# Kernel tuning notes

Measured on AMD Instinct MI355X. Metric: run time of the kernel, lower is better.

## Reference

```python
import jax, jax.numpy as jnp
import numpy as np


def setup_inputs() -> dict:
    key = jax.random.key(0)
    k1, k2 = jax.random.split(key)
    B, S, D = 4, 2048, 1024
    x = jax.random.normal(k1, (B, S, D), dtype=jnp.float32)
    # uniform initializer in keras is small; scale to keep softmax well-behaved
    kernel = jax.random.normal(k2, (3, D, D), dtype=jnp.float32) * 0.02
    return {"x": x, "kernel": kernel}


def reference(x, kernel):
    # x: [B, S, D], kernel: [3, D, D]
    D = x.shape[-1]
    q = jnp.einsum('bsd,de->bse', x, kernel[0])
    k = jnp.einsum('bsd,de->bse', x, kernel[1])
    v = jnp.einsum('bsd,de->bse', x, kernel[2])
    scores = jnp.einsum('bqe,bke->bqk', q, k) / jnp.sqrt(jnp.float32(D))
    attn = jax.nn.softmax(scores, axis=-1)
    return jnp.einsum('bqk,bke->bqe', attn, v)
```

## Files before the change

### kernel.cpp

```cpp
#include <hip/hip_runtime.h>
#include <hip/hip_bf16.h>
#include <cstdint>

typedef __bf16 bf16x8 __attribute__((ext_vector_type(8)));
typedef float f32x4 __attribute__((ext_vector_type(4)));

__device__ __forceinline__ unsigned short f2bf(float f) {
  union { float f; uint32_t u; } a; a.f = f;
  uint32_t r = a.u + 0x7fffu + ((a.u >> 16) & 1u);
  return (unsigned short)(r >> 16);
}
__device__ __forceinline__ void gload_lds16(const unsigned short* g, unsigned short* l) {
  __builtin_amdgcn_global_load_lds(
      (const __attribute__((address_space(1))) void*)g,
      (__attribute__((address_space(3))) void*)l, 16, 0, 0);
}

__global__ void cast_all(const float* __restrict__ x, const float* __restrict__ W,
                         unsigned short* __restrict__ xb, unsigned short* __restrict__ Wt) {
  __shared__ float tile[32][33];
  const int bx = blockIdx.x;
  const int t = threadIdx.x;
  if (bx < 4096) {
    size_t i = ((size_t)bx * 256 + t) * 8;
    float4 a = *(const float4*)(x + i);
    float4 b = *(const float4*)(x + i + 4);
    uint4 o;
    o.x = (uint32_t)f2bf(a.x) | ((uint32_t)f2bf(a.y) << 16);
    o.y = (uint32_t)f2bf(a.z) | ((uint32_t)f2bf(a.w) << 16);
    o.z = (uint32_t)f2bf(b.x) | ((uint32_t)f2bf(b.y) << 16);
    o.w = (uint32_t)f2bf(b.z) | ((uint32_t)f2bf(b.w) << 16);
    *(uint4*)(xb + i) = o;
  } else {
    const int b = bx - 4096;
    const int z = b >> 10;
    const int rest = b & 1023;
    const int bxx = rest & 31, byy = rest >> 5;
    const float* Wz = W + (size_t)z * 1048576;
    unsigned short* Wtz = Wt + (size_t)z * 1048576;
    const int x0 = bxx * 32, y0 = byy * 32;
    const int tx = t & 31, ty = t >> 5;
#pragma unroll
    for (int i = 0; i < 32; i += 8)
      tile[ty + i][tx] = Wz[(size_t)(y0 + ty + i) * 1024 + x0 + tx];
    __syncthreads();
#pragma unroll
    for (int i = 0; i < 32; i += 8)
      Wtz[(size_t)(x0 + ty + i) * 1024 + y0 + tx] = f2bf(tile[tx][ty + i]);
  }
}

template <int MODE>
__global__ void __launch_bounds__(256)
gemm_bt(const unsigned short* __restrict__ Aall,
        const unsigned short* __restrict__ Btall,
        void* __restrict__ Call, unsigned short* __restrict__ VtPtr,
        float* __restrict__ aux,
        int K, int ldc, long sA, long sB, long sC, float scale) {
  __shared__ unsigned short As[2][4096];
  __shared__ unsigned short Bs[2][4096];
  const int t = threadIdx.x;
  const int lane = t & 63;
  const int quad = lane >> 4;
  const int l15 = lane & 15;
  const int wave = t >> 6;
  const int wm = (wave >> 1) * 64;
  const int wn = (wave & 1) * 64;
  const int z = blockIdx.z;

  const unsigned short* A = Aall + (size_t)z * sA + (size_t)blockIdx.x * 128 * K;
  const unsigned short* Bt = Btall + (size_t)z * sB + (size_t)blockIdx.y * 128 * K;

  const int srow = t >> 2;
  const int scol = (((t & 3) ^ ((srow >> 1) & 3)) * 8);
  const unsigned short* ga = A + (size_t)srow * K + scol;
  const unsigned short* gb = Bt + (size_t)srow * K + scol;
  const size_t rowskip = (size_t)64 * K;

  const int aOff = (wm + l15) * 32 + (quad ^ ((l15 >> 1) & 3)) * 8;
  const int bOff = (wn + l15) * 32 + (quad ^ ((l15 >> 1) & 3)) * 8;

  f32x4 acc[4][4];
#pragma unroll
  for (int i = 0; i < 4; i++)
#pragma unroll
    for (int j = 0; j < 4; j++) acc[i][j] = (f32x4){0.f, 0.f, 0.f, 0.f};

  gload_lds16(ga, &As[0][t * 8]);
  gload_lds16(ga + rowskip, &As[0][2048 + t * 8]);
  gload_lds16(gb, &Bs[0][t * 8]);
  gload_lds16(gb + rowskip, &Bs[0][2048 + t * 8]);

  int buf = 0;
  for (int k0 = 0; k0 < K; k0 += 32, buf ^= 1) {
    __syncthreads();
    if (k0 + 32 < K) {
      const int kn = k0 + 32;
      gload_lds16(ga + kn, &As[buf ^ 1][t * 8]);
      gload_lds16(ga + rowskip + kn, &As[buf ^ 1][2048 + t * 8]);
      gload_lds16(gb + kn, &Bs[buf ^ 1][t * 8]);
      gload_lds16(gb + rowskip + kn, &Bs[buf ^ 1][2048 + t * 8]);
    }
    const unsigned short* aB = &As[buf][aOff];
    const unsigned short* bB = &Bs[buf][bOff];
    bf16x8 a[4], b[4];
#pragma unroll
    for (int i = 0; i < 4; i++) a[i] = *(const bf16x8*)(aB + i * 512);
#pragma unroll
    for (int j = 0; j < 4; j++) b[j] = *(const bf16x8*)(bB + j * 512);
#pragma unroll
    for (int i = 0; i < 4; i++)
#pragma unroll
      for (int j = 0; j < 4; j++)
        acc[i][j] = __builtin_amdgcn_mfma_f32_16x16x32_bf16(a[i], b[j], acc[i][j], 0, 0, 0);
  }

  const int mbase = blockIdx.x * 128 + wm + quad * 4;
  const int nbase = blockIdx.y * 128 + wn + l15;

  if (MODE == 4) {
    if (z < 2) {
      unsigned short* C = (unsigned short*)Call + (size_t)z * sC;
#pragma unroll
      for (int mi = 0; mi < 4; mi++)
#pragma unroll
        for (int ni = 0; ni < 4; ni++) {
          const int m = mbase + mi * 16, n = nbase + ni * 16;
#pragma unroll
          for (int r = 0; r < 4; r++)
            C[(size_t)(m + r) * ldc + n] = f2bf(acc[mi][ni][r]);
        }
    } else {
      unsigned short* C = VtPtr;
#pragma unroll
      for (int mi = 0; mi < 4; mi++) {
        const int m = mbase + mi * 16;
        const int b = m >> 11, s = m & 2047;
#pragma unroll
        for (int ni = 0; ni < 4; ni++) {
          const int n = nbase + ni * 16;
          uint2 val;
          val.x = (uint32_t)f2bf(acc[mi][ni][0]) | ((uint32_t)f2bf(acc[mi][ni][1]) << 16);
          val.y = (uint32_t)f2bf(acc[mi][ni][2]) | ((uint32_t)f2bf(acc[mi][ni][3]) << 16);
          *(uint2*)(C + (size_t)b * 2097152 + (size_t)n * 2048 + s) = val;
        }
      }
    }
  } else if (MODE == 5) {
    unsigned short* C = (unsigned short*)Call + (size_t)z * sC;
    const int j = blockIdx.y * 2 + (wn >> 6);
#pragma unroll
    for (int mi = 0; mi < 4; mi++) {
#pragma unroll
      for (int r = 0; r < 4; r++) {
        const int m = mbase + mi * 16 + r;
        float s = 0.f;
#pragma unroll
        for (int ni = 0; ni < 4; ni++) {
          const float e = __expf(acc[mi][ni][r] * scale);
          C[(size_t)m * ldc + nbase + ni * 16] = f2bf(e);
          s += e;
        }
        s += __shfl_xor(s, 1);
        s += __shfl_xor(s, 2);
        s += __shfl_xor(s, 4);
        s += __shfl_xor(s, 8);
        if (l15 == 0) aux[(size_t)j * 8192 + (size_t)z * 2048 + m] = s;
      }
    }
  } else {
    float* C = (float*)Call + (size_t)z * sC;
#pragma unroll
    for (int mi = 0; mi < 4; mi++) {
#pragma unroll
      for (int r = 0; r < 4; r++) {
        const int m = mbase + mi * 16 + r;
        const size_t grow = (size_t)z * 2048 + m;
        float tot = 0.f;
#pragma unroll
        for (int j = 0; j < 32; j++) tot += aux[(size_t)j * 8192 + grow];
        const float inv = 1.f / tot;
#pragma unroll
        for (int ni = 0; ni < 4; ni++)
          C[(size_t)m * ldc + nbase + ni * 16] = acc[mi][ni][r] * inv;
      }
    }
  }
}

extern "C" void kernel_launch(void* const* d_in, const int* in_sizes, int n_in,
                              void* d_out, int out_size, void* d_ws, size_t ws_size,
                              hipStream_t stream) {
  const float* x = (const float*)d_in[0];
  const float* W = (const float*)d_in[1];
  float* out = (float*)d_out;
  char* ws = (char*)d_ws;
  unsigned short* xb = (unsigned short*)(ws);
  unsigned short* Wt = (unsigned short*)(ws + (16ll << 20));
  float* partial     = (float*)(ws + (16ll << 20));
  unsigned short* Q  = (unsigned short*)(ws + (22ll << 20));
  unsigned short* Kb = (unsigned short*)(ws + (38ll << 20));
  unsigned short* Vt = (unsigned short*)(ws + (54ll << 20));
  unsigned short* Sb = (unsigned short*)(ws + (70ll << 20));

  cast_all<<<7168, 256, 0, stream>>>(x, W, xb, Wt);

  gemm_bt<4><<<dim3(64, 8, 3), 256, 0, stream>>>(
      xb, Wt, Q, Vt, nullptr, 1024, 1024, 0L, 1048576L, 8388608L, 1.0f);
  gemm_bt<5><<<dim3(16, 16, 4), 256, 0, stream>>>(
      Q, Kb, Sb, nullptr, partial, 1024, 2048, 2097152L, 2097152L, 4194304L, 0.03125f);
  gemm_bt<6><<<dim3(16, 8, 4), 256, 0, stream>>>(
      Sb, Vt, out, nullptr, partial, 2048, 1024, 4194304L, 2097152L, 2097152L, 1.0f);
}
```

Baseline: 263.4 us.

## Fuse all attention stages into one cooperative persistent kernel with grid syncs

```diff
diff --git a/kernel.cpp b/kernel.cpp
--- a/kernel.cpp
+++ b/kernel.cpp
@@ -1,9 +1,17 @@
 #include <hip/hip_runtime.h>
+#include <hip/hip_cooperative_groups.h>
 #include <hip/hip_bf16.h>
 #include <cstdint>
 
+namespace cg = cooperative_groups;
+
 typedef __bf16 bf16x8 __attribute__((ext_vector_type(8)));
 typedef float f32x4 __attribute__((ext_vector_type(4)));
+
+struct SharedMem {
+  unsigned short As[2][4096];
+  unsigned short Bs[2][4096];
+};
 
 __device__ __forceinline__ unsigned short f2bf(float f) {
   union { float f; uint32_t u; } a; a.f = f;
@@ -16,60 +24,17 @@
       (__attribute__((address_space(3))) void*)l, 16, 0, 0);
 }
 
-__global__ void cast_all(const float* __restrict__ x, const float* __restrict__ W,
-                         unsigned short* __restrict__ xb, unsigned short* __restrict__ Wt) {
-  __shared__ float tile[32][33];
-  const int bx = blockIdx.x;
-  const int t = threadIdx.x;
-  if (bx < 4096) {
-    size_t i = ((size_t)bx * 256 + t) * 8;
-    float4 a = *(const float4*)(x + i);
-    float4 b = *(const float4*)(x + i + 4);
-    uint4 o;
-    o.x = (uint32_t)f2bf(a.x) | ((uint32_t)f2bf(a.y) << 16);
-    o.y = (uint32_t)f2bf(a.z) | ((uint32_t)f2bf(a.w) << 16);
-    o.z = (uint32_t)f2bf(b.x) | ((uint32_t)f2bf(b.y) << 16);
-    o.w = (uint32_t)f2bf(b.z) | ((uint32_t)f2bf(b.w) << 16);
-    *(uint4*)(xb + i) = o;
-  } else {
-    const int b = bx - 4096;
-    const int z = b >> 10;
-    const int rest = b & 1023;
-    const int bxx = rest & 31, byy = rest >> 5;
-    const float* Wz = W + (size_t)z * 1048576;
-    unsigned short* Wtz = Wt + (size_t)z * 1048576;
-    const int x0 = bxx * 32, y0 = byy * 32;
-    const int tx = t & 31, ty = t >> 5;
-#pragma unroll
-    for (int i = 0; i < 32; i += 8)
-      tile[ty + i][tx] = Wz[(size_t)(y0 + ty + i) * 1024 + x0 + tx];
-    __syncthreads();
-#pragma unroll
-    for (int i = 0; i < 32; i += 8)
-      Wtz[(size_t)(x0 + ty + i) * 1024 + y0 + tx] = f2bf(tile[tx][ty + i]);
-  }
-}
-
-template <int MODE>
-__global__ void __launch_bounds__(256)
-gemm_bt(const unsigned short* __restrict__ Aall,
-        const unsigned short* __restrict__ Btall,
-        void* __restrict__ Call, unsigned short* __restrict__ VtPtr,
-        float* __restrict__ aux,
-        int K, int ldc, long sA, long sB, long sC, float scale) {
-  __shared__ unsigned short As[2][4096];
-  __shared__ unsigned short Bs[2][4096];
+template <int NJ>
+__device__ __forceinline__ void gemm_tile_core(
+    const unsigned short* __restrict__ A, const unsigned short* __restrict__ Bt,
+    int K, SharedMem& sh, f32x4 (&acc)[4][NJ]) {
   const int t = threadIdx.x;
   const int lane = t & 63;
   const int quad = lane >> 4;
   const int l15 = lane & 15;
   const int wave = t >> 6;
   const int wm = (wave >> 1) * 64;
-  const int wn = (wave & 1) * 64;
-  const int z = blockIdx.z;
-
-  const unsigned short* A = Aall + (size_t)z * sA + (size_t)blockIdx.x * 128 * K;
-  const unsigned short* Bt = Btall + (size_t)z * sB + (size_t)blockIdx.y * 128 * K;
+  const int wn = (wave & 1) * (NJ * 16);
 
   const int srow = t >> 2;
   const int scol = (((t & 3) ^ ((srow >> 1) & 3)) * 8);
@@ -77,50 +42,104 @@
   const unsigned short* gb = Bt + (size_t)srow * K + scol;
   const size_t rowskip = (size_t)64 * K;
 
-  const int aOff = (wm + l15) * 32 + (quad ^ ((l15 >> 1) & 3)) * 8;
-  const int bOff = (wn + l15) * 32 + (quad ^ ((l15 >> 1) & 3)) * 8;
-
-  f32x4 acc[4][4];
+  const int swz = (quad ^ ((l15 >> 1) & 3)) * 8;
+  const int aOff = (wm + l15) * 32 + swz;
+  const int bOff = (wn + l15) * 32 + swz;
+
 #pragma unroll
   for (int i = 0; i < 4; i++)
 #pragma unroll
-    for (int j = 0; j < 4; j++) acc[i][j] = (f32x4){0.f, 0.f, 0.f, 0.f};
-
-  gload_lds16(ga, &As[0][t * 8]);
-  gload_lds16(ga + rowskip, &As[0][2048 + t * 8]);
-  gload_lds16(gb, &Bs[0][t * 8]);
-  gload_lds16(gb + rowskip, &Bs[0][2048 + t * 8]);
+    for (int j = 0; j < NJ; j++) acc[i][j] = (f32x4){0.f, 0.f, 0.f, 0.f};
+
+  gload_lds16(ga, &sh.As[0][t * 8]);
+  gload_lds16(ga + rowskip, &sh.As[0][2048 + t * 8]);
+  gload_lds16(gb, &sh.Bs[0][t * 8]);
+  if (NJ == 4) gload_lds16(gb + rowskip, &sh.Bs[0][2048 + t * 8]);
 
   int buf = 0;
   for (int k0 = 0; k0 < K; k0 += 32, buf ^= 1) {
     __syncthreads();
     if (k0 + 32 < K) {
       const int kn = k0 + 32;
-      gload_lds16(ga + kn, &As[buf ^ 1][t * 8]);
-      gload_lds16(ga + rowskip + kn, &As[buf ^ 1][2048 + t * 8]);
-      gload_lds16(gb + kn, &Bs[buf ^ 1][t * 8]);
-      gload_lds16(gb + rowskip + kn, &Bs[buf ^ 1][2048 + t * 8]);
+      gload_lds16(ga + kn, &sh.As[buf ^ 1][t * 8]);
+      gload_lds16(ga + rowskip + kn, &sh.As[buf ^ 1][2048 + t * 8]);
+      gload_lds16(gb + kn, &sh.Bs[buf ^ 1][t * 8]);
+      if (NJ == 4) gload_lds16(gb + rowskip + kn, &sh.Bs[buf ^ 1][2048 + t * 8]);
     }
-    const unsigned short* aB = &As[buf][aOff];
-    const unsigned short* bB = &Bs[buf][bOff];
-    bf16x8 a[4], b[4];
+    const unsigned short* aB = &sh.As[buf][aOff];
+    const unsigned short* bB = &sh.Bs[buf][bOff];
+    bf16x8 a[4], b[NJ];
 #pragma unroll
     for (int i = 0; i < 4; i++) a[i] = *(const bf16x8*)(aB + i * 512);
 #pragma unroll
-    for (int j = 0; j < 4; j++) b[j] = *(const bf16x8*)(bB + j * 512);
+    for (int j = 0; j < NJ; j++) b[j] = *(const bf16x8*)(bB + j * 512);
 #pragma unroll
     for (int i = 0; i < 4; i++)
 #pragma unroll
-      for (int j = 0; j < 4; j++)
+      for (int j = 0; j < NJ; j++)
         acc[i][j] = __builtin_amdgcn_mfma_f32_16x16x32_bf16(a[i], b[j], acc[i][j], 0, 0, 0);
   }
-
-  const int mbase = blockIdx.x * 128 + wm + quad * 4;
-  const int nbase = blockIdx.y * 128 + wn + l15;
-
-  if (MODE == 4) {
+}
+
+
+__device__ __forceinline__ void phase0_casts(const float* __restrict__ x,
+                                             const float* __restrict__ W,
+                                             unsigned short* __restrict__ xb,
+                                             unsigned short* __restrict__ Wt,
+                                             SharedMem& sh) {
+  const int bid = blockIdx.x, t = threadIdx.x;
+#pragma unroll
+  for (int i = 0; i < 4; i++) {
+    size_t idx = (((size_t)(bid + i * 1024)) * 256 + t) * 8;
+    float4 a = *(const float4*)(x + idx);
+    float4 b = *(const float4*)(x + idx + 4);
+    uint4 o;
+    o.x = (uint32_t)f2bf(a.x) | ((uint32_t)f2bf(a.y) << 16);
+    o.y = (uint32_t)f2bf(a.z) | ((uint32_t)f2bf(a.w) << 16);
+    o.z = (uint32_t)f2bf(b.x) | ((uint32_t)f2bf(b.y) << 16);
+    o.w = (uint32_t)f2bf(b.z) | ((uint32_t)f2bf(b.w) << 16);
+    *(uint4*)(xb + idx) = o;
+  }
+  float* tile = (float*)sh.As;
+  const int tx = t & 31, ty = t >> 5;
+  for (int i = 0; i < 3; i++) {
+    const int u = bid + i * 1024;
+    const int z = u >> 10, rest = u & 1023;
+    const float* Wz = W + (size_t)z * 1048576;
+    unsigned short* Wtz = Wt + (size_t)z * 1048576;
+    const int x0 = (rest & 31) * 32, y0 = (rest >> 5) * 32;
+#pragma unroll
+    for (int ii = 0; ii < 32; ii += 8)
+      tile[(ty + ii) * 33 + tx] = Wz[(size_t)(y0 + ty + ii) * 1024 + x0 + tx];
+    __syncthreads();
+#pragma unroll
+    for (int ii = 0; ii < 32; ii += 8)
+      Wtz[(size_t)(x0 + ty + ii) * 1024 + y0 + tx] = f2bf(tile[tx * 33 + ty + ii]);
+    __syncthreads();
+  }
+}
+
+__device__ __forceinline__ void phase1_qkv(const unsigned short* __restrict__ xb,
+                                           const unsigned short* __restrict__ Wt,
+                                           unsigned short* __restrict__ Q,
+                                           unsigned short* __restrict__ Kb,
+                                           unsigned short* __restrict__ Vt,
+                                           SharedMem& sh) {
+  const int t = threadIdx.x;
+  const int lane = t & 63, quad = lane >> 4, l15 = lane & 15, wave = t >> 6;
+  const int wm = (wave >> 1) * 64;
+  for (int pass = 0; pass < 2; pass++) {
+    const int v = blockIdx.x + pass * 1024;
+    if (v >= 1536) break;
+    const int z = v >> 9, mt = (v >> 3) & 63, nt = v & 7;
+    const unsigned short* A = xb + (size_t)mt * 128 * 1024;
+    const unsigned short* Bt = Wt + (size_t)z * 1048576 + (size_t)nt * 128 * 1024;
+    f32x4 acc[4][4];
+    gemm_tile_core<4>(A, Bt, 1024, sh, acc);
+    const int mbase = mt * 128 + wm + quad * 4;
+    const int nbase = nt * 128 + (wave & 1) * 64 + l15;
     if (z < 2) {
-      unsigned short* C = (unsigned short*)Call + (size_t)z * sC;
+      unsigned short* C = (z == 0) ? Q : Kb;
 #pragma unroll
       for (int mi = 0; mi < 4; mi++)
 #pragma unroll
@@ -128,10 +147,9 @@
           const int m = mbase + mi * 16, n = nbase + ni * 16;
 #pragma unroll
           for (int r = 0; r < 4; r++)
-            C[(size_t)(m + r) * ldc + n] = f2bf(acc[mi][ni][r]);
+            C[(size_t)(m + r) * 1024 + n] = f2bf(acc[mi][ni][r]);
         }
     } else {
-      unsigned short* C = VtPtr;
 #pragma unroll
       for (int mi = 0; mi < 4; mi++) {
         const int m = mbase + mi * 16;
@@ -142,50 +160,130 @@
           uint2 val;
           val.x = (uint32_t)f2bf(acc[mi][ni][0]) | ((uint32_t)f2bf(acc[mi][ni][1]) << 16);
           val.y = (uint32_t)f2bf(acc[mi][ni][2]) | ((uint32_t)f2bf(acc[mi][ni][3]) << 16);
-          *(uint2*)(C + (size_t)b * 2097152 + (size_t)n * 2048 + s) = val;
+          *(uint2*)(Vt + (size_t)b * 2097152 + (size_t)n * 2048 + s) = val;
         }
       }
     }
-  } else if (MODE == 5) {
-    unsigned short* C = (unsigned short*)Call + (size_t)z * sC;
-    const int j = blockIdx.y * 2 + (wn >> 6);
-#pragma unroll
-    for (int mi = 0; mi < 4; mi++) {
-#pragma unroll
-      for (int r = 0; r < 4; r++) {
-        const int m = mbase + mi * 16 + r;
-        float s = 0.f;
-#pragma unroll
-        for (int ni = 0; ni < 4; ni++) {
-          const float e = __expf(acc[mi][ni][r] * scale);
-          C[(size_t)m * ldc + nbase + ni * 16] = f2bf(e);
-          s += e;
-        }
-        s += __shfl_xor(s, 1);
-        s += __shfl_xor(s, 2);
-        s += __shfl_xor(s, 4);
-        s += __shfl_xor(s, 8);
-        if (l15 == 0) aux[(size_t)j * 8192 + (size_t)z * 2048 + m] = s;
+  }
+}
+
+__device__ __forceinline__ void phase2_scores(const unsigned short* __restrict__ Q,
+                                              const unsigned short* __restrict__ Kb,
+                                              unsigned short* __restrict__ Sb,
+                                              float* __restrict__ partial,
+                                              SharedMem& sh) {
+  const int t = threadIdx.x;
+  const int lane = t & 63, quad = lane >> 4, l15 = lane & 15, wave = t >> 6;
+  const int wm = (wave >> 1) * 64;
+  const int v = blockIdx.x;
+  const int z = v >> 8, mt = (v >> 4) & 15, nt = v & 15;
+  const unsigned short* A = Q + (size_t)z * 2097152 + (size_t)mt * 128 * 1024;
+  const unsigned short* Bt = Kb + (size_t)z * 2097152 + (size_t)nt * 128 * 1024;
+  f32x4 acc[4][4];
+  gemm_tile_core<4>(A, Bt, 1024, sh, acc);
+  unsigned short* C = Sb + (size_t)z * 4194304;
+  const int mbase = mt * 128 + wm + quad * 4;
+  const int nbase = nt * 128 + (wave & 1) * 64 + l15;
+  const int j = nt * 2 + (wave & 1);
+#pragma unroll
+  for (int mi = 0; mi < 4; mi++) {
+#pragma unroll
+    for (int r = 0; r < 4; r++) {
+      const int m = mbase + mi * 16 + r;
+      float s = 0.f;
+#pragma unroll
+      for (int ni = 0; ni < 4; ni++) {
+        const float e = __expf(acc[mi][ni][r] * 0.03125f);
+        C[(size_t)m * 2048 + nbase + ni * 16] = f2bf(e);
+        s += e;
       }
+      s += __shfl_xor(s, 1);
+      s += __shfl_xor(s, 2);
+      s += __shfl_xor(s, 4);
+      s += __shfl_xor(s, 8);
+      if (l15 == 0) partial[(size_t)j * 8192 + (size_t)z * 2048 + m] = s;
     }
-  } else {
-    float* C = (float*)Call + (size_t)z * sC;
-#pragma unroll
-    for (int mi = 0; mi < 4; mi++) {
-#pragma unroll
-      for (int r = 0; r < 4; r++) {
-        const int m = mbase + mi * 16 + r;
-        const size_t grow = (size_t)z * 2048 + m;
-        float tot = 0.f;
-#pragma unroll
-        for (int j = 0; j < 32; j++) tot += aux[(size_t)j * 8192 + grow];
-        const float inv = 1.f / tot;
-#pragma unroll
-        for (int ni = 0; ni < 4; ni++)
-          C[(size_t)m * ldc + nbase + ni * 16] = acc[mi][ni][r] * inv;
-      }
+  }
+}
+
+__device__ __forceinline__ void phase3_pv(const unsigned short* __restrict__ Sb,
+                                          const unsigned short* __restrict__ Vt,
+                                          const float* __restrict__ partial,
+                                          float* __restrict__ out,
+                                          SharedMem& sh) {
+  const int t = threadIdx.x;
+  const int lane = t & 63, quad = lane >> 4, l15 = lane & 15, wave = t >> 6;
+  const int wm = (wave >> 1) * 64;
+  const int v = blockIdx.x;
+  const int z = v >> 8, mt = (v >> 4) & 15, et = v & 15;
+  const unsigned short* A = Sb + (size_t)z * 4194304 + (size_t)mt * 128 * 2048;
+  const unsigned short* Bt = Vt + (size_t)z * 2097152 + (size_t)et * 64 * 2048;
+  f32x4 acc[4][2];
+  gemm_tile_core<2>(A, Bt, 2048, sh, acc);
+  __syncthreads();
+  float* rowinv = (float*)sh.As;
+  if (t < 128) {
+    const size_t grow = (size_t)z * 2048 + mt * 128 + t;
+    float s = 0.f;
+#pragma unroll 8
+    for (int j = 0; j < 32; j++) s += partial[(size_t)j * 8192 + grow];
+    rowinv[t] = 1.f / s;
+  }
+  __syncthreads();
+  float* C = out + (size_t)z * 2097152;
+  const int mbase = mt * 128 + wm + quad * 4;
+  const int nbase = et * 64 + (wave & 1) * 32 + l15;
+#pragma unroll
+  for (int mi = 0; mi < 4; mi++) {
+#pragma unroll
+    for (int r = 0; r < 4; r++) {
+      const int m = mbase + mi * 16 + r;
+      const float inv = rowinv[m & 127];
+#pragma unroll
+      for (int ni = 0; ni < 2; ni++)
+        C[(size_t)m * 1024 + nbase + ni * 16] = acc[mi][ni][r] * inv;
     }
   }
+}
+
+__global__ void __launch_bounds__(256, 4)
+fused_attn(const float* __restrict__ x, const float* __restrict__ W,
+           float* __restrict__ out, char* __restrict__ ws) {
+  __shared__ SharedMem sh;
+  unsigned short* xb = (unsigned short*)(ws);
+  unsigned short* Wt = (unsigned short*)(ws + (16ll << 20));
+  float* partial     = (float*)(ws + (16ll << 20));
+  unsigned short* Q  = (unsigned short*)(ws + (22ll << 20));
+  unsigned short* Kb = (unsigned short*)(ws + (38ll << 20));
+  unsigned short* Vt = (unsigned short*)(ws + (54ll << 20));
+  unsigned short* Sb = (unsigned short*)(ws + (70ll << 20));
+  cg::grid_group grid = cg::this_grid();
+
+  phase0_casts(x, W, xb, Wt, sh);
+  grid.sync();
+  phase1_qkv(xb, Wt, Q, Kb, Vt, sh);
+  grid.sync();
+  phase2_scores(Q, Kb, Sb, partial, sh);
+  grid.sync();
+  phase3_pv(Sb, Vt, partial, out, sh);
+}
+
+template <int P>
+__global__ void __launch_bounds__(256)
+phase_kernel(const float* __restrict__ x, const float* __restrict__ W,
+             float* __restrict__ out, char* __restrict__ ws) {
+  __shared__ SharedMem sh;
+  unsigned short* xb = (unsigned short*)(ws);
+  unsigned short* Wt = (unsigned short*)(ws + (16ll << 20));
+  float* partial     = (float*)(ws + (16ll << 20));
+  unsigned short* Q  = (unsigned short*)(ws + (22ll << 20));
+  unsigned short* Kb = (unsigned short*)(ws + (38ll << 20));
+  unsigned short* Vt = (unsigned short*)(ws + (54ll << 20));
+  unsigned short* Sb = (unsigned short*)(ws + (70ll << 20));
+  if (P == 0) phase0_casts(x, W, xb, Wt, sh);
+  else if (P == 1) phase1_qkv(xb, Wt, Q, Kb, Vt, sh);
+  else if (P == 2) phase2_scores(Q, Kb, Sb, partial, sh);
+  else phase3_pv(Sb, Vt, partial, out, sh);
 }
 
 extern "C" void kernel_launch(void* const* d_in, const int* in_sizes, int n_in,
@@ -195,20 +293,20 @@
   const float* W = (const float*)d_in[1];
   float* out = (float*)d_out;
   char* ws = (char*)d_ws;
-  unsigned short* xb = (unsigned short*)(ws);
-  unsigned short* Wt = (unsigned short*)(ws + (16ll << 20));
-  float* partial     = (float*)(ws + (16ll << 20));
-  unsigned short* Q  = (unsigned short*)(ws + (22ll << 20));
-  unsigned short* Kb = (unsigned short*)(ws + (38ll << 20));
-  unsigned short* Vt = (unsigned short*)(ws + (54ll << 20));
-  unsigned short* Sb = (unsigned short*)(ws + (70ll << 20));
-
-  cast_all<<<7168, 256, 0, stream>>>(x, W, xb, Wt);
-
-  gemm_bt<4><<<dim3(64, 8, 3), 256, 0, stream>>>(
-      xb, Wt, Q, Vt, nullptr, 1024, 1024, 0L, 1048576L, 8388608L, 1.0f);
-  gemm_bt<5><<<dim3(16, 16, 4), 256, 0, stream>>>(
-      Q, Kb, Sb, nullptr, partial, 1024, 2048, 2097152L, 2097152L, 4194304L, 0.03125f);
-  gemm_bt<6><<<dim3(16, 8, 4), 256, 0, stream>>>(
-      Sb, Vt, out, nullptr, partial, 2048, 1024, 4194304L, 2097152L, 2097152L, 1.0f);
-}
+
+  int nb = 0;
+  bool coop =
+      (hipOccupancyMaxActiveBlocksPerMultiprocessor(&nb, (const void*)fused_attn, 256, 0) ==
+       hipSuccess) && nb >= 4;
+  if (coop) {
+    void* args[] = {(void*)&x, (void*)&W, (void*)&out, (void*)&ws};
+    coop = (hipLaunchCooperativeKernel((void*)fused_attn, dim3(1024), dim3(256), args, 0,
+                                       stream) == hipSuccess);
+  }
+  if (!coop) {
+    phase_kernel<0><<<1024, 256, 0, stream>>>(x, W, out, ws);
+    phase_kernel<1><<<1024, 256, 0, stream>>>(x, W, out, ws);
+    phase_kernel<2><<<1024, 256, 0, stream>>>(x, W, out, ws);
+    phase_kernel<3><<<1024, 256, 0, stream>>>(x, W, out, ws);
+  }
+}
```

New measurement: 291.1 us. 10.5% more time.
